# Kernel optimization log

Measured on AMD Instinct MI355X. Metric: run time of the kernel, lower is better.

## Reference

```python
import jax, jax.numpy as jnp
import numpy as np

EPS = 1e-8  # torch F.cosine_similarity norm clamp


def setup_inputs() -> dict:
    key = jax.random.key(0)
    k1, k2, k3, k4 = jax.random.split(key, 4)
    B, N, M, D, T = 8, 4096, 2048, 512, 2
    return {
        "features": jax.random.normal(k1, (B, N, D), dtype=jnp.float32),
        "text": jax.random.normal(k2, (T, M, D), dtype=jnp.float32),
        "W": jax.random.normal(k3, (D, D), dtype=jnp.float32) * 0.02,
        "b": jax.random.normal(k4, (D,), dtype=jnp.float32) * 0.02,
    }


def reference(features, text, W, b):
    # features: [B, N, D] (output of the extractor), text: [T, M, D]
    B, N, D = features.shape
    f1 = jnp.einsum("bnd,de->bne", features, W) + b  # linear_layer(features)
    t1 = text[1]  # [M, D]; expanded across batch (row 1 per original code)

    # cosine similarity over last dim without materializing [B, N, M, D]
    fn = f1 / jnp.maximum(jnp.linalg.norm(f1, axis=-1, keepdims=True), EPS)
    tn = t1 / jnp.maximum(jnp.linalg.norm(t1, axis=-1, keepdims=True), EPS)
    sim = jnp.einsum("bnd,md->bnm", fn, tn)  # [B, N, M]

    e = jnp.exp(sim)
    w = e / jnp.sum(e, axis=1, keepdims=True)  # normalize over N (dim=1)

    # features_t [B,D,N] @ w [B,N,M] -> [B,D,M] -> transpose -> [B,M,D]
    fm = jnp.einsum("bnd,bnm->bmd", features, w)

    t1b = jnp.broadcast_to(t1[None, :, :], (B,) + t1.shape)  # [B, M, D]
    combine_feature = jnp.concatenate([fm, t1b], axis=2)  # [B, M, 2D]
    return combine_feature
```

## Files before the change

### kernel.cpp

```cpp
#include <hip/hip_runtime.h>

#define B_SZ 8
#define N_SZ 4096
#define M_SZ 2048
#define D_SZ 512

typedef __attribute__((ext_vector_type(8))) short bf16x8;
typedef __attribute__((ext_vector_type(4))) float f32x4;
typedef __attribute__((address_space(1))) const void* gptr1;
typedef __attribute__((address_space(3))) void* lptr3;

__device__ __forceinline__ unsigned short f2bf(float x) {
    unsigned int u = __builtin_bit_cast(unsigned int, x);
    u += 0x7fffu + ((u >> 16) & 1u);
    return (unsigned short)(u >> 16);
}

__device__ __forceinline__ void bt_mainloop(
    const unsigned short* __restrict__ A, const unsigned short* __restrict__ Bt,
    int lda, int ldb, int rowBase, int colBase, int K,
    unsigned short* As, unsigned short* Bs, f32x4 acc[4][4])
{
    const int tid  = threadIdx.x;
    const int lane = tid & 63;
    const int w    = tid >> 6;
    const int wr   = (w >> 1) * 64;
    const int wc   = (w & 1) * 64;
    const int lr   = lane & 15;
    const int kq   = lane >> 4;

    const int srow0 = w * 16 + (lane >> 2);
    const int skk   = (lane & 3) * 8;

    for (int k0 = 0; k0 < K; k0 += 32) {
#pragma unroll
        for (int j = 0; j < 2; ++j) {
            const unsigned short* ga = A  + (size_t)(rowBase + srow0 + j * 64) * lda + (k0 + skk);
            const unsigned short* gb = Bt + (size_t)(colBase + srow0 + j * 64) * ldb + (k0 + skk);
            __builtin_amdgcn_global_load_lds((gptr1)ga, (lptr3)(As + (j * 4 + w) * 512), 16, 0, 0);
            __builtin_amdgcn_global_load_lds((gptr1)gb, (lptr3)(Bs + (j * 4 + w) * 512), 16, 0, 0);
        }
        asm volatile("s_waitcnt vmcnt(0)" ::: "memory");
        __syncthreads();

        bf16x8 af[4], bq[4];
#pragma unroll
        for (int i = 0; i < 4; ++i) {
            af[i] = *(const bf16x8*)(As + (wr + i * 16 + lr) * 32 + kq * 8);
            bq[i] = *(const bf16x8*)(Bs + (wc + i * 16 + lr) * 32 + kq * 8);
        }
#pragma unroll
        for (int mi = 0; mi < 4; ++mi)
#pragma unroll
            for (int ni = 0; ni < 4; ++ni)
                acc[mi][ni] = __builtin_amdgcn_mfma_f32_16x16x32_bf16(af[mi], bq[ni], acc[mi][ni], 0, 0, 0);
        __syncthreads();
    }
}

__global__ __launch_bounds__(256) void prep_t_k(
    const float* __restrict__ text, const float* __restrict__ bias,
    unsigned short* __restrict__ t1bf, float* __restrict__ invs, float* __restrict__ c2,
    float* __restrict__ out, float* __restrict__ L, float* __restrict__ SS)
{
    const int m = blockIdx.x;
    const int t = threadIdx.x;
    const float* t1 = text + (size_t)M_SZ * D_SZ;
    float2 v = ((const float2*)(t1 + (size_t)m * D_SZ))[t];
    float2 bb = ((const float2*)bias)[t];
    float s = v.x * v.x + v.y * v.y;
    float c = v.x * bb.x + v.y * bb.y;
#pragma unroll
    for (int off = 32; off > 0; off >>= 1) { s += __shfl_down(s, off); c += __shfl_down(c, off); }
    __shared__ float ps[4], pc[4];
    if ((t & 63) == 0) { ps[t >> 6] = s; pc[t >> 6] = c; }
    __syncthreads();
    if (t == 0) {
        float norm = fmaxf(sqrtf(ps[0] + ps[1] + ps[2] + ps[3]), 1e-8f);
        invs[m] = 1.f / norm;
        c2[m] = pc[0] + pc[1] + pc[2] + pc[3];
    }
    ushort2 pk; pk.x = f2bf(v.x); pk.y = f2bf(v.y);
    ((ushort2*)(t1bf + (size_t)m * D_SZ))[t] = pk;
#pragma unroll
    for (int b = 0; b < B_SZ; ++b) {
        ((float2*)(out + ((size_t)(b * M_SZ + m)) * (2 * D_SZ) + D_SZ))[t] = v;
        ((float2*)(out + ((size_t)(b * M_SZ + m)) * (2 * D_SZ)))[t] = (float2){0.f, 0.f};
    }
    if (m < 64) L[m * 256 + t] = 0.f;
    if (m < 128) SS[m * 256 + t] = 0.f;
}

__global__ __launch_bounds__(256) void prep_w_k(
    const float* __restrict__ W, unsigned short* __restrict__ Wt,
    unsigned short* __restrict__ Wbf)
{
    const int dt = blockIdx.x, et = blockIdx.y;
    const int t = threadIdx.x;
    __shared__ unsigned short tile[64][72];
    const int rr = t >> 4;
    const int cc = (t & 15) * 4;
#pragma unroll
    for (int p = 0; p < 4; ++p) {
        const int d = p * 16 + rr;
        const float4 v = *(const float4*)(W + (size_t)(dt * 64 + d) * D_SZ + et * 64 + cc);
        ushort4 pk; pk.x = f2bf(v.x); pk.y = f2bf(v.y); pk.z = f2bf(v.z); pk.w = f2bf(v.w);
        *(ushort4*)(Wbf + (size_t)(dt * 64 + d) * D_SZ + et * 64 + cc) = pk;
        tile[d][cc] = pk.x; tile[d][cc + 1] = pk.y; tile[d][cc + 2] = pk.z; tile[d][cc + 3] = pk.w;
    }
    __syncthreads();
#pragma unroll
    for (int p = 0; p < 4; ++p) {
        const int e = p * 16 + rr;
        ushort4 pk;
        pk.x = tile[cc][e]; pk.y = tile[cc + 1][e]; pk.z = tile[cc + 2][e]; pk.w = tile[cc + 3][e];
        *(ushort4*)(Wt + (size_t)(et * 64 + e) * D_SZ + dt * 64 + cc) = pk;
    }
}

__global__ __launch_bounds__(256) void convert_feat_k(
    const float* __restrict__ feat, unsigned short* __restrict__ V,
    unsigned short* __restrict__ Vt)
{
    const int nt = blockIdx.x, dt = blockIdx.y, b = blockIdx.z;
    const int t = threadIdx.x;
    __shared__ unsigned short tile[64][72];
    const int rr = t >> 4;
    const int cc = (t & 15) * 4;
#pragma unroll
    for (int p = 0; p < 4; ++p) {
        const int r = p * 16 + rr;
        const size_t grow = (size_t)(b * N_SZ + nt * 64 + r);
        const float4 v = *(const float4*)(feat + grow * D_SZ + dt * 64 + cc);
        ushort4 pk; pk.x = f2bf(v.x); pk.y = f2bf(v.y); pk.z = f2bf(v.z); pk.w = f2bf(v.w);
        *(ushort4*)(V + grow * D_SZ + dt * 64 + cc) = pk;
        tile[r][cc] = pk.x; tile[r][cc + 1] = pk.y; tile[r][cc + 2] = pk.z; tile[r][cc + 3] = pk.w;
    }
    __syncthreads();
#pragma unroll
    for (int p = 0; p < 4; ++p) {
        const int d = p * 16 + rr;
        ushort4 pk;
        pk.x = tile[cc][d]; pk.y = tile[cc + 1][d]; pk.z = tile[cc + 2][d]; pk.w = tile[cc + 3][d];
        *(ushort4*)(Vt + ((size_t)(b * D_SZ + dt * 64 + d)) * N_SZ + nt * 64 + cc) = pk;
    }
}

__global__ __launch_bounds__(256) void gemm1f_k(
    const unsigned short* __restrict__ V, const unsigned short* __restrict__ Wt,
    const float* __restrict__ bias, float* __restrict__ SS,
    const unsigned short* __restrict__ t1bf, const unsigned short* __restrict__ Wbf,
    unsigned short* __restrict__ ttn)
{
    __shared__ unsigned short As[128 * 32];
    __shared__ unsigned short Bs[128 * 32];
    f32x4 acc[4][4];
#pragma unroll
    for (int i = 0; i < 4; ++i)
#pragma unroll
        for (int j = 0; j < 4; ++j) acc[i][j] = (f32x4){0.f, 0.f, 0.f, 0.f};
    const int tid = threadIdx.x, lane = tid & 63, w = tid >> 6;
    const int wr = (w >> 1) * 64, wc = (w & 1) * 64, lr = lane & 15, kq = lane >> 4;
    const int blk = blockIdx.x;

    if (blk < 64) {
        const int rowBase = (blk >> 2) * 128;
        const int colBase = (blk & 3) * 128;
        bt_mainloop(t1bf, Wbf, D_SZ, D_SZ, rowBase, colBase, D_SZ, As, Bs, acc);
#pragma unroll
        for (int mi = 0; mi < 4; ++mi) {
            const int r0 = rowBase + wr + mi * 16 + kq * 4;
#pragma unroll
            for (int ni = 0; ni < 4; ++ni) {
                const int c = colBase + wc + ni * 16 + lr;
#pragma unroll
                for (int r = 0; r < 4; ++r)
                    ttn[(size_t)(r0 + r) * D_SZ + c] = f2bf(acc[mi][ni][r]);
            }
        }
    } else {
        const int bb = blk - 64;
        const int rowBase = (bb >> 2) * 128;
        const int colBase = (bb & 3) * 128;
        bt_mainloop(V, Wt, D_SZ, D_SZ, rowBase, colBase, D_SZ, As, Bs, acc);
#pragma unroll
        for (int mi = 0; mi < 4; ++mi) {
            const int r0 = rowBase + wr + mi * 16 + kq * 4;
            float s[4] = {0.f, 0.f, 0.f, 0.f};
#pragma unroll
            for (int ni = 0; ni < 4; ++ni) {
                const int c = colBase + wc + ni * 16 + lr;
                const float bv = bias[c];
#pragma unroll
                for (int r = 0; r < 4; ++r) {
                    const float v = acc[mi][ni][r] + bv;
                    s[r] += v * v;
                }
            }
#pragma unroll
            for (int off = 1; off <= 8; off <<= 1)
#pragma unroll
                for (int r = 0; r < 4; ++r) s[r] += __shfl_xor(s[r], off);
            if (lr == 0) {
#pragma unroll
                for (int r = 0; r < 4; ++r) atomicAdd(&SS[r0 + r], s[r]);
            }
        }
    }
}

__global__ __launch_bounds__(256) void gemm2_k(
    const unsigned short* __restrict__ V, const unsigned short* __restrict__ ttn,
    const float* __restrict__ SS, const float* __restrict__ invs,
    const float* __restrict__ c2, unsigned short* __restrict__ E,
    float* __restrict__ L)
{
    __shared__ unsigned short smem[128 * 136];
    unsigned short* As = smem;
    unsigned short* Bs = smem + 4096;
    f32x4 acc[4][4];
#pragma unroll
    for (int i = 0; i < 4; ++i)
#pragma unroll
        for (int j = 0; j < 4; ++j) acc[i][j] = (f32x4){0.f, 0.f, 0.f, 0.f};
    const int tid = threadIdx.x, lane = tid & 63, w = tid >> 6;
    const int wr = (w >> 1) * 64, wc = (w & 1) * 64, lr = lane & 15, kq = lane >> 4;

    const int lin = blockIdx.x;
    const int xcd = lin & 7, slot = lin >> 3;
    const int mt = slot & 15;
    const int rt = (slot >> 4) * 8 + xcd;
    const int rowBase = rt * 128;
    const int colBase = mt * 128;

    bt_mainloop(V, ttn, D_SZ, D_SZ, rowBase, colBase, D_SZ, As, Bs, acc);

    const int b  = rowBase >> 12;
    const int nb = rowBase & 4095;
    unsigned short* Eb = E + (size_t)b * M_SZ * N_SZ;
    unsigned short* P = smem;

    float invr[4][4];
#pragma unroll
    for (int mi = 0; mi < 4; ++mi) {
        const int r0 = rowBase + wr + mi * 16 + kq * 4;
#pragma unroll
        for (int r = 0; r < 4; ++r)
            invr[mi][r] = 1.f / fmaxf(sqrtf(SS[r0 + r]), 1e-8f);
    }

#pragma unroll
    for (int ni = 0; ni < 4; ++ni) {
        const int mm = wc + ni * 16 + lr;
        const float sm = invs[colBase + mm];
        const float cm = c2[colBase + mm];
        float p = 0.f;
#pragma unroll
        for (int mi = 0; mi < 4; ++mi) {
            const int nn0 = wr + mi * 16 + kq * 4;
            const float e0 = __expf((acc[mi][ni][0] + cm) * invr[mi][0] * sm);
            const float e1 = __expf((acc[mi][ni][1] + cm) * invr[mi][1] * sm);
            const float e2 = __expf((acc[mi][ni][2] + cm) * invr[mi][2] * sm);
            const float e3 = __expf((acc[mi][ni][3] + cm) * invr[mi][3] * sm);
            ushort4 pk; pk.x = f2bf(e0); pk.y = f2bf(e1); pk.z = f2bf(e2); pk.w = f2bf(e3);
            *(ushort4*)(P + mm * 136 + nn0) = pk;
            p += (e0 + e1) + (e2 + e3);
        }
        p += __shfl_down(p, 16);
        p += __shfl_down(p, 32);
        if (lane < 16) atomicAdd(&L[b * M_SZ + colBase + mm], p);
    }
    __syncthreads();

    const int tr = tid >> 4;
    const int tc = (tid & 15) * 8;
#pragma unroll
    for (int j = 0; j < 8; ++j) {
        const int mm = j * 16 + tr;
        bf16x8 v = *(const bf16x8*)(P + mm * 136 + tc);
        *(bf16x8*)(Eb + (size_t)(colBase + mm) * N_SZ + nb + tc) = v;
    }
}

__global__ __launch_bounds__(256) void gemm3_k(
    const unsigned short* __restrict__ E, const unsigned short* __restrict__ Vt,
    const float* __restrict__ L, float* __restrict__ out)
{
    __shared__ unsigned short As[128 * 32];
    __shared__ unsigned short Bs[128 * 32];
    f32x4 acc[4][4];
#pragma unroll
    for (int i = 0; i < 4; ++i)
#pragma unroll
        for (int j = 0; j < 4; ++j) acc[i][j] = (f32x4){0.f, 0.f, 0.f, 0.f};
    const int tid = threadIdx.x, lane = tid & 63, w = tid >> 6;
    const int wr = (w >> 1) * 64, wc = (w & 1) * 64, lr = lane & 15, kq = lane >> 4;

    const int lin = blockIdx.x;
    const int dt = lin >> 8;
    const int g  = lin & 255;
    const int b  = g >> 5;
    const int mt = (g & 31) >> 1;
    const int kh = g & 1;

    const int rowBase = mt * 128;
    const int colBase = dt * 128;
    const unsigned short* Ab = E  + (size_t)b * M_SZ * N_SZ + (size_t)kh * 2048;
    const unsigned short* Bb = Vt + (size_t)b * D_SZ * N_SZ + (size_t)kh * 2048;
    bt_mainloop(Ab, Bb, N_SZ, N_SZ, rowBase, colBase, 2048, As, Bs, acc);

#pragma unroll
    for (int mi = 0; mi < 4; ++mi) {
        const int r0 = rowBase + wr + mi * 16 + kq * 4;
        float invl[4];
#pragma unroll
        for (int r = 0; r < 4; ++r) invl[r] = 1.f / L[b * M_SZ + r0 + r];
#pragma unroll
        for (int ni = 0; ni < 4; ++ni) {
            const int d = colBase + wc + ni * 16 + lr;
#pragma unroll
            for (int r = 0; r < 4; ++r)
                atomicAdd(&out[((size_t)(b * M_SZ + r0 + r)) * (2 * D_SZ) + d],
                          acc[mi][ni][r] * invl[r]);
        }
    }
}

extern "C" void kernel_launch(void* const* d_in, const int* in_sizes, int n_in,
                              void* d_out, int out_size, void* d_ws, size_t ws_size,
                              hipStream_t stream) {
    const float* features = (const float*)d_in[0];
    const float* text     = (const float*)d_in[1];
    const float* W        = (const float*)d_in[2];
    const float* bias     = (const float*)d_in[3];
    float* out = (float*)d_out;
    char* ws = (char*)d_ws;

    unsigned short* t1bf = (unsigned short*)(ws + 0);
    unsigned short* ttn  = (unsigned short*)(ws + 2097152);
    unsigned short* Wt   = (unsigned short*)(ws + 4194304);
    unsigned short* Wbf  = (unsigned short*)(ws + 4718592);
    unsigned short* V    = (unsigned short*)(ws + 5242880);
    unsigned short* Vt   = (unsigned short*)(ws + 38797312);
    float*          L    = (float*)(ws + 72351744);
    float*          SS   = (float*)(ws + 72417280);
    float*          invs = (float*)(ws + 72548352);
    float*          c2   = (float*)(ws + 72556544);
    unsigned short* E    = (unsigned short*)(ws + 72564736);

    hipLaunchKernelGGL(prep_t_k, dim3(M_SZ), dim3(256), 0, stream,
                       text, bias, t1bf, invs, c2, out, L, SS);
    hipLaunchKernelGGL(prep_w_k, dim3(8, 8), dim3(256), 0, stream, W, Wt, Wbf);
    hipLaunchKernelGGL(convert_feat_k, dim3(64, 8, 8), dim3(256), 0, stream, features, V, Vt);
    hipLaunchKernelGGL(gemm1f_k, dim3(1088), dim3(256), 0, stream,
                       V, Wt, bias, SS, t1bf, Wbf, ttn);
    hipLaunchKernelGGL(gemm2_k, dim3(4096), dim3(256), 0, stream,
                       V, ttn, SS, invs, c2, E, L);
    hipLaunchKernelGGL(gemm3_k, dim3(1024), dim3(256), 0, stream, E, Vt, L, out);
}
```

Before: 419.6 us.

## Replace split-K atomic output accumulation with partial buffers and last-block reduction

The final GEMM no longer zero-initialises the output half and atomically adds each split-K half into it. Each block now writes its fp32 partial tile to a workspace buffer that reuses the space of the dead V array. A per-tile counter then elects the second-arriving block, which adds its sibling's partial, applies the 1/L scaling and does plain stores. The block index mapping is also reordered so batch varies fastest, and the workspace layout is reshuffled. This removes float atomics and the zero-fill writes, at the cost of an extra partial write and read plus threadfence synchronisation.

After: 605.3 us. +44.3%, slower.

```diff
diff --git a/kernel.cpp b/kernel.cpp
--- a/kernel.cpp
+++ b/kernel.cpp
@@ -61,7 +61,8 @@
 __global__ __launch_bounds__(256) void prep_t_k(
     const float* __restrict__ text, const float* __restrict__ bias,
     unsigned short* __restrict__ t1bf, float* __restrict__ invs, float* __restrict__ c2,
-    float* __restrict__ out, float* __restrict__ L, float* __restrict__ SS)
+    float* __restrict__ out, float* __restrict__ L, float* __restrict__ SS,
+    unsigned int* __restrict__ flags)
 {
     const int m = blockIdx.x;
     const int t = threadIdx.x;
@@ -83,12 +84,11 @@
     ushort2 pk; pk.x = f2bf(v.x); pk.y = f2bf(v.y);
     ((ushort2*)(t1bf + (size_t)m * D_SZ))[t] = pk;
 #pragma unroll
-    for (int b = 0; b < B_SZ; ++b) {
+    for (int b = 0; b < B_SZ; ++b)
         ((float2*)(out + ((size_t)(b * M_SZ + m)) * (2 * D_SZ) + D_SZ))[t] = v;
-        ((float2*)(out + ((size_t)(b * M_SZ + m)) * (2 * D_SZ)))[t] = (float2){0.f, 0.f};
-    }
     if (m < 64) L[m * 256 + t] = 0.f;
     if (m < 128) SS[m * 256 + t] = 0.f;
+    if (m < 2) flags[m * 256 + t] = 0u;
 }
 
 __global__ __launch_bounds__(256) void prep_w_k(
@@ -284,10 +284,12 @@
 
 __global__ __launch_bounds__(256) void gemm3_k(
     const unsigned short* __restrict__ E, const unsigned short* __restrict__ Vt,
-    const float* __restrict__ L, float* __restrict__ out)
+    const float* __restrict__ L, float* __restrict__ Ppart,
+    unsigned int* __restrict__ flags, float* __restrict__ out)
 {
     __shared__ unsigned short As[128 * 32];
     __shared__ unsigned short Bs[128 * 32];
+    __shared__ int winner;
     f32x4 acc[4][4];
 #pragma unroll
     for (int i = 0; i < 4; ++i)
@@ -297,11 +299,11 @@
     const int wr = (w >> 1) * 64, wc = (w & 1) * 64, lr = lane & 15, kq = lane >> 4;
 
     const int lin = blockIdx.x;
-    const int dt = lin >> 8;
-    const int g  = lin & 255;
-    const int b  = g >> 5;
-    const int mt = (g & 31) >> 1;
-    const int kh = g & 1;
+    const int b  = lin & 7;
+    const int s  = lin >> 3;
+    const int mt = s >> 3;
+    const int dt = (s >> 1) & 3;
+    const int kh = s & 1;
 
     const int rowBase = mt * 128;
     const int colBase = dt * 128;
@@ -309,19 +311,43 @@
     const unsigned short* Bb = Vt + (size_t)b * D_SZ * N_SZ + (size_t)kh * 2048;
     bt_mainloop(Ab, Bb, N_SZ, N_SZ, rowBase, colBase, 2048, As, Bs, acc);
 
+    const int pid = (b * 16 + mt) * 4 + dt;
+    float* myP = Ppart + ((size_t)pid * 2 + kh) * (128 * 128);
+
 #pragma unroll
     for (int mi = 0; mi < 4; ++mi) {
-        const int r0 = rowBase + wr + mi * 16 + kq * 4;
+        const int rr0 = wr + mi * 16 + kq * 4;
+#pragma unroll
+        for (int ni = 0; ni < 4; ++ni) {
+            const int cc = wc + ni * 16 + lr;
+#pragma unroll
+            for (int r = 0; r < 4; ++r)
+                myP[(size_t)(rr0 + r) * 128 + cc] = acc[mi][ni][r];
+        }
+    }
+    __threadfence();
+    __syncthreads();
+    if (tid == 0) winner = (int)atomicAdd(&flags[pid], 1u);
+    __syncthreads();
+    if (winner == 0) return;
+    __threadfence();
+
+    const float* sibP = Ppart + ((size_t)pid * 2 + (1 - kh)) * (128 * 128);
+#pragma unroll
+    for (int mi = 0; mi < 4; ++mi) {
+        const int rr0 = wr + mi * 16 + kq * 4;
         float invl[4];
 #pragma unroll
-        for (int r = 0; r < 4; ++r) invl[r] = 1.f / L[b * M_SZ + r0 + r];
+        for (int r = 0; r < 4; ++r) invl[r] = 1.f / L[b * M_SZ + rowBase + rr0 + r];
 #pragma unroll
         for (int ni = 0; ni < 4; ++ni) {
-            const int d = colBase + wc + ni * 16 + lr;
-#pragma unroll
-            for (int r = 0; r < 4; ++r)
-                atomicAdd(&out[((size_t)(b * M_SZ + r0 + r)) * (2 * D_SZ) + d],
-                          acc[mi][ni][r] * invl[r]);
+            const int cc = wc + ni * 16 + lr;
+#pragma unroll
+            for (int r = 0; r < 4; ++r) {
+                const float v = acc[mi][ni][r] + sibP[(size_t)(rr0 + r) * 128 + cc];
+                out[((size_t)(b * M_SZ + rowBase + rr0 + r)) * (2 * D_SZ) + colBase + cc] =
+                    v * invl[r];
+            }
         }
     }
 }
@@ -336,25 +362,28 @@
     float* out = (float*)d_out;
     char* ws = (char*)d_ws;
 
-    unsigned short* t1bf = (unsigned short*)(ws + 0);
-    unsigned short* ttn  = (unsigned short*)(ws + 2097152);
-    unsigned short* Wt   = (unsigned short*)(ws + 4194304);
-    unsigned short* Wbf  = (unsigned short*)(ws + 4718592);
-    unsigned short* V    = (unsigned short*)(ws + 5242880);
-    unsigned short* Vt   = (unsigned short*)(ws + 38797312);
-    float*          L    = (float*)(ws + 72351744);
-    float*          SS   = (float*)(ws + 72417280);
-    float*          invs = (float*)(ws + 72548352);
-    float*          c2   = (float*)(ws + 72556544);
-    unsigned short* E    = (unsigned short*)(ws + 72564736);
+    unsigned short* V    = (unsigned short*)(ws + 0);
+    unsigned short* t1bf = (unsigned short*)(ws + 33554432);
+    unsigned short* ttn  = (unsigned short*)(ws + 35651584);
+    unsigned short* Wt   = (unsigned short*)(ws + 37748736);
+    unsigned short* Wbf  = (unsigned short*)(ws + 38273024);
+    float*          Ppart= (float*)(ws + 0);
+    unsigned short* Vt   = (unsigned short*)(ws + 67108864);
+    float*          L    = (float*)(ws + 100663296);
+    float*          SS   = (float*)(ws + 100728832);
+    float*          invs = (float*)(ws + 100859904);
+    float*          c2   = (float*)(ws + 100868096);
+    unsigned int*   flags= (unsigned int*)(ws + 100876288);
+    unsigned short* E    = (unsigned short*)(ws + 100878336);
 
     hipLaunchKernelGGL(prep_t_k, dim3(M_SZ), dim3(256), 0, stream,
-                       text, bias, t1bf, invs, c2, out, L, SS);
+                       text, bias, t1bf, invs, c2, out, L, SS, flags);
     hipLaunchKernelGGL(prep_w_k, dim3(8, 8), dim3(256), 0, stream, W, Wt, Wbf);
     hipLaunchKernelGGL(convert_feat_k, dim3(64, 8, 8), dim3(256), 0, stream, features, V, Vt);
     hipLaunchKernelGGL(gemm1f_k, dim3(1088), dim3(256), 0, stream,
                        V, Wt, bias, SS, t1bf, Wbf, ttn);
     hipLaunchKernelGGL(gemm2_k, dim3(4096), dim3(256), 0, stream,
                        V, ttn, SS, invs, c2, E, L);
-    hipLaunchKernelGGL(gemm3_k, dim3(1024), dim3(256), 0, stream, E, Vt, L, out);
-}
+    hipLaunchKernelGGL(gemm3_k, dim3(1024), dim3(256), 0, stream,
+                       E, Vt, L, Ppart, flags, out);
+}
```
